# Optimization experiments

Hardware: AMD Instinct MI355X
Metric: run time of the kernel (lower is better)

Reference implementation:

```python
import jax, jax.numpy as jnp
import numpy as np

NC = 80
T0, T1 = 0.0025, 0.0225  # scale_area_thresholds
BOX_W, OBJ_W, CLS_W = 5.0, 1.0, 1.0
BOOST = 2.0  # small_object_boost


def setup_inputs() -> dict:
    key = jax.random.key(0)
    ks = jax.random.split(key, 9)
    B, A, T = 16, 3, 100
    grids = [(80, 80), (40, 40), (20, 20)]
    outs = [jax.random.normal(ks[i], (B, A, h, w, 5 + NC), jnp.float32)
            for i, (h, w) in enumerate(grids)]
    # targets: [B, T, 5] = (x1, y1, x2, y2, class_id) in normalized coords
    cx = jax.random.uniform(ks[3], (B, T), minval=0.05, maxval=0.95)
    cy = jax.random.uniform(ks[4], (B, T), minval=0.05, maxval=0.95)
    # log-uniform sides -> areas span both thresholds (all 3 scales hit)
    bw = 10.0 ** jax.random.uniform(ks[5], (B, T), minval=-2.3, maxval=-0.6)
    bh = 10.0 ** jax.random.uniform(ks[6], (B, T), minval=-2.3, maxval=-0.6)
    cls_id = jnp.floor(jax.random.uniform(ks[7], (B, T)) * NC)
    targets = jnp.stack([cx - bw / 2, cy - bh / 2, cx + bw / 2, cy + bh / 2, cls_id], axis=-1).astype(jnp.float32)
    return {"out0": outs[0], "out1": outs[1], "out2": outs[2], "targets": targets}


def _bce(logits, t):
    # BCEWithLogits: log(1+e^x) - x*t, numerically stable via logaddexp
    return jnp.logaddexp(0.0, logits) - logits * t


def _iou_xyxy(b1, b2, eps=1e-6):
    x1 = jnp.maximum(b1[..., 0], b2[..., 0]); y1 = jnp.maximum(b1[..., 1], b2[..., 1])
    x2 = jnp.minimum(b1[..., 2], b2[..., 2]); y2 = jnp.minimum(b1[..., 3], b2[..., 3])
    inter = jnp.clip(x2 - x1, 0.0) * jnp.clip(y2 - y1, 0.0)
    a1 = jnp.clip(b1[..., 2] - b1[..., 0], 0.0) * jnp.clip(b1[..., 3] - b1[..., 1], 0.0)
    a2 = jnp.clip(b2[..., 2] - b2[..., 0], 0.0) * jnp.clip(b2[..., 3] - b2[..., 1], 0.0)
    return inter / (a1 + a2 - inter + eps)


def _build_targets(tgts, scale_index, A, H, W):
    """Sequential (order-faithful) scatter of GT boxes onto the grid; vmapped over batch."""
    def per_image(tg):  # tg: [T, 5]
        init = (jnp.zeros((H, W), jnp.float32), jnp.zeros((H, W, 4), jnp.float32),
                jnp.zeros((H, W, NC), jnp.float32), jnp.ones((H, W), jnp.float32))

        def step(carry, t):
            obj, box, cls, w = carry
            x1 = jnp.clip(t[0], 0.0, 1.0); y1 = jnp.clip(t[1], 0.0, 1.0)
            x2 = jnp.clip(t[2], 0.0, 1.0); y2 = jnp.clip(t[3], 0.0, 1.0)
            valid = (x2 > x1) & (y2 > y1)
            area = (x2 - x1) * (y2 - y1)
            sidx = jnp.where(area <= T0, 0, jnp.where(area <= T1, 1, 2))
            valid = valid & (sidx == scale_index)
            gi = jnp.clip(jnp.floor(0.5 * (x1 + x2) * W).astype(jnp.int32), 0, W - 1)
            gj = jnp.clip(jnp.floor(0.5 * (y1 + y2) * H).astype(jnp.int32), 0, H - 1)
            cid = t[4].astype(jnp.int32)
            cls_ok = (cid >= 0) & (cid < NC)
            cidc = jnp.clip(cid, 0, NC - 1)
            smallness = 1.0 - jnp.minimum(1.0, area / max(T0, 1e-6))
            weight = 1.0 + (BOOST - 1.0) * jnp.maximum(0.0, smallness)
            bvec = jnp.stack([x1, y1, x2, y2])
            obj = obj.at[gj, gi].set(jnp.where(valid, 1.0, obj[gj, gi]))
            box = box.at[gj, gi].set(jnp.where(valid, bvec, box[gj, gi]))
            cls = cls.at[gj, gi, cidc].set(jnp.where(valid & cls_ok, 1.0, cls[gj, gi, cidc]))
            w = w.at[gj, gi].set(jnp.where(valid, weight, w[gj, gi]))
            tiny = valid & (area <= T0)
            for dj, di in ((-1, 0), (1, 0), (0, -1), (0, 1)):
                nj, ni = gj + dj, gi + di
                ok = tiny & (nj >= 0) & (nj < H) & (ni >= 0) & (ni < W)
                njc = jnp.clip(nj, 0, H - 1); nic = jnp.clip(ni, 0, W - 1)
                obj = obj.at[njc, nic].set(jnp.where(ok, jnp.maximum(obj[njc, nic], 0.5), obj[njc, nic]))
                box = box.at[njc, nic].set(jnp.where(ok, bvec, box[njc, nic]))
                cls = cls.at[njc, nic, cidc].set(jnp.where(ok & cls_ok, 1.0, cls[njc, nic, cidc]))
                w = w.at[njc, nic].set(jnp.where(ok, jnp.maximum(w[njc, nic], 0.5 * weight), w[njc, nic]))
            return (obj, box, cls, w), None

        (obj, box, cls, w), _ = jax.lax.scan(step, init, tg)
        return obj, box, cls, w

    obj, box, cls, w = jax.vmap(per_image)(tgts)
    B = tgts.shape[0]
    # only anchor 0 is ever assigned (anchor_id = 0 in the original)
    obj_f = jnp.zeros((B, A, H, W), jnp.float32).at[:, 0].set(obj)
    box_f = jnp.zeros((B, A, H, W, 4), jnp.float32).at[:, 0].set(box)
    cls_f = jnp.zeros((B, A, H, W, NC), jnp.float32).at[:, 0].set(cls)
    w_f = jnp.ones((B, A, H, W), jnp.float32).at[:, 0].set(w)
    return obj_f, box_f, cls_f, w_f


def _scale_loss(out, tgts, scale_index):
    B, A, H, W, _ = out.shape
    reg, objp, clsp = out[..., :4], out[..., 4], out[..., 5:]
    obj_t, box_t, cls_t, sw = _build_targets(tgts, scale_index, A, H, W)
    obj_loss = _bce(objp, obj_t).mean()
    pos = obj_t > 0.5
    npos = jnp.sum(pos)
    denom = jnp.maximum(npos, 1).astype(jnp.float32)
    pb = jax.nn.sigmoid(reg)
    d = pb - box_t
    ad = jnp.abs(d)
    l1 = jnp.where(ad < 1.0, 0.5 * d * d, ad - 0.5).mean(-1)  # smooth_l1, beta=1
    box_per = (l1 + 1.0 - _iou_xyxy(pb, box_t)) * sw
    box_loss = jnp.where(npos > 0, jnp.sum(jnp.where(pos, box_per, 0.0)) / denom, 0.0)
    cls_per = _bce(clsp, cls_t).mean(-1) * sw
    cls_loss = jnp.where(npos > 0, jnp.sum(jnp.where(pos, cls_per, 0.0)) / denom, 0.0)
    return box_loss, obj_loss, cls_loss


def reference(out0, out1, out2, targets):
    targets = jax.lax.stop_gradient(targets)  # torch builds targets from python floats (detached)
    outs = (out0, out1, out2)
    bl = ol = cl = 0.0
    for s, o in enumerate(outs):
        b, ob, c = _scale_loss(o, targets, s)
        bl, ol, cl = bl + b, ol + ob, cl + c
    n = float(len(outs))
    bl, ol, cl = bl / n, ol / n, cl / n
    final = BOX_W * bl + OBJ_W * ol + CLS_W * cl
    return final, bl, ol, cl
```

## Files before the change

kernel.cpp:

```cpp
#include <hip/hip_runtime.h>
#include <math.h>

#define NCLS 80
#define NB 16
#define NA 3
#define NT 100

static constexpr int TOTCELLS  = 134400;
static constexpr int CELL_OFF1 = 102400;
static constexpr int CELL_OFF2 = 128000;

static constexpr int OBJ_TOT  = 403200;
static constexpr int OBJ_OFF1 = 307200;
static constexpr int OBJ_OFF2 = 384000;

__device__ unsigned g_lastMain[TOTCELLS];
__device__ unsigned g_lastAny [TOTCELLS];
__device__ unsigned g_maskA   [TOTCELLS*3];
__device__ float4   g_bvec  [NB*NT];
__device__ float    g_weight[NB*NT];
__device__ double   g_objsum[3];
__device__ double   g_boxsum[3];
__device__ double   g_clssum[3];
__device__ unsigned g_npos  [3];
__device__ unsigned g_posCount;
__device__ unsigned g_posList[NB*NT];

__device__ __forceinline__ float softplusf(float x) {
    return fmaxf(x, 0.0f) + log1pf(expf(-fabsf(x)));
}

__global__ __launch_bounds__(256) void k_clear() {
    int i = blockIdx.x * 256 + threadIdx.x;
    g_lastMain[i] = 0u;
    g_lastAny[i]  = 0u;
    g_maskA[3*i+0] = 0u; g_maskA[3*i+1] = 0u; g_maskA[3*i+2] = 0u;
    if (i < 3) { g_objsum[i] = 0.0; g_boxsum[i] = 0.0; g_clssum[i] = 0.0; g_npos[i] = 0u; }
    if (i == 0) g_posCount = 0u;
}

__global__ __launch_bounds__(256) void k_scatter(const float* __restrict__ tgt) {
    int idx = blockIdx.x * 256 + threadIdx.x;
    if (idx >= NB * NT) return;
    int b = idx / NT, t = idx % NT;
    const float* p = tgt + (size_t)idx * 5;
    float x1 = fminf(fmaxf(p[0], 0.0f), 1.0f);
    float y1 = fminf(fmaxf(p[1], 0.0f), 1.0f);
    float x2 = fminf(fmaxf(p[2], 0.0f), 1.0f);
    float y2 = fminf(fmaxf(p[3], 0.0f), 1.0f);
    bool valid = (x2 > x1) && (y2 > y1);
    float area = (x2 - x1) * (y2 - y1);
    int sidx = (area <= 0.0025f) ? 0 : ((area <= 0.0225f) ? 1 : 2);
    int Wd = (sidx == 0) ? 80 : ((sidx == 1) ? 40 : 20);
    int HWc = Wd * Wd;
    int soff = (sidx == 0) ? 0 : ((sidx == 1) ? CELL_OFF1 : CELL_OFF2);

    int gi = (int)floorf(0.5f * (x1 + x2) * (float)Wd);
    int gj = (int)floorf(0.5f * (y1 + y2) * (float)Wd);
    gi = min(max(gi, 0), Wd - 1);
    gj = min(max(gj, 0), Wd - 1);

    int cid = (int)p[4];
    bool cls_ok = (cid >= 0) && (cid < NCLS);
    float smallness = 1.0f - fminf(1.0f, area / 0.0025f);
    float weight = 1.0f + fmaxf(0.0f, smallness);

    g_bvec[idx]   = make_float4(x1, y1, x2, y2);
    g_weight[idx] = weight;

    if (!valid) return;
    unsigned seq = (unsigned)(t + 1);
    int cell = soff + b * HWc + gj * Wd + gi;
    atomicMax(&g_lastMain[cell], seq);
    atomicMax(&g_lastAny[cell],  seq);
    if (cls_ok) atomicOr(&g_maskA[3*cell + (cid >> 5)], 1u << (cid & 31));

    if (area <= 0.0025f) {
        const int dj[4] = {-1, 1, 0, 0};
        const int di[4] = {0, 0, -1, 1};
        #pragma unroll
        for (int k = 0; k < 4; ++k) {
            int nj = gj + dj[k], ni = gi + di[k];
            if (nj >= 0 && nj < Wd && ni >= 0 && ni < Wd) {
                int nc = soff + b * HWc + nj * Wd + ni;
                atomicMax(&g_lastAny[nc], seq);
                if (cls_ok) atomicOr(&g_maskA[3*nc + (cid >> 5)], 1u << (cid & 31));
            }
        }
    }
}

__global__ __launch_bounds__(256) void k_obj(const float* __restrict__ o0,
                                             const float* __restrict__ o1,
                                             const float* __restrict__ o2) {
    __shared__ double sred[256];
    int n = blockIdx.x * 256 + threadIdx.x;
    int s, loc, HW, soff;
    const float* out;
    if (n < OBJ_OFF1)      { s = 0; loc = n;            out = o0; HW = 6400; soff = 0; }
    else if (n < OBJ_OFF2) { s = 1; loc = n - OBJ_OFF1; out = o1; HW = 1600; soff = CELL_OFF1; }
    else                   { s = 2; loc = n - OBJ_OFF2; out = o2; HW = 400;  soff = CELL_OFF2; }
    int b = loc / (NA * HW);
    int r = loc % (NA * HW);
    int a = r / HW;
    int cij = r % HW;

    float x = out[(size_t)loc * 85 + 4];
    float contrib = softplusf(x);
    if (a == 0) {
        int cell = soff + b * HW + cij;
        unsigned lm = g_lastMain[cell];
        float tv = lm ? 1.0f : (g_lastAny[cell] ? 0.5f : 0.0f);
        contrib -= x * tv;
        if (lm) {
            unsigned slot = atomicAdd(&g_posCount, 1u);
            g_posList[slot] = (unsigned)cell;
            atomicAdd(&g_npos[s], 1u);
        }
    }
    sred[threadIdx.x] = (double)contrib;
    __syncthreads();
    for (int st = 128; st > 0; st >>= 1) {
        if (threadIdx.x < st) sred[threadIdx.x] += sred[threadIdx.x + st];
        __syncthreads();
    }
    if (threadIdx.x == 0) atomicAdd(&g_objsum[s], sred[0]);
}

__global__ __launch_bounds__(256) void k_poswork(const float* __restrict__ o0,
                                                 const float* __restrict__ o1,
                                                 const float* __restrict__ o2) {
    __shared__ double sB[4], sC[4];
    __shared__ int    sS[4];
    int wv   = threadIdx.x >> 6;
    int lane = threadIdx.x & 63;
    int w = blockIdx.x * 4 + wv;
    unsigned count = g_posCount;

    double bsum = 0.0, csum = 0.0;
    int sidx = -1;
    if (w < (int)count) {
        int n = (int)g_posList[w];
        int s, b, cij, HW;
        const float* out;
        if (n < CELL_OFF1)      { s = 0; HW = 6400; int l = n;             b = l / 6400; cij = l % 6400; out = o0; }
        else if (n < CELL_OFF2) { s = 1; HW = 1600; int l = n - CELL_OFF1; b = l / 1600; cij = l % 1600; out = o1; }
        else                    { s = 2; HW = 400;  int l = n - CELL_OFF2; b = l / 400;  cij = l % 400;  out = o2; }
        sidx = s;

        const float* base = out + ((size_t)(b * NA * HW) + (size_t)cij) * 85;
        float v0 = base[lane];
        float v1 = (lane < 21) ? base[64 + lane] : 0.0f;

        unsigned m0 = g_maskA[3*n], m1 = g_maskA[3*n+1], m2 = g_maskA[3*n+2];
        unsigned lm = g_lastMain[n], la = g_lastAny[n];
        float4 bt = g_bvec[b * NT + (int)(la - 1u)];
        float  sw = g_weight[b * NT + (int)(lm - 1u)];

        float cl_ = 0.0f;
        if (lane >= 5) {
            int c = lane - 5;
            unsigned bit = ((c < 32) ? (m0 >> c) : (m1 >> (c - 32))) & 1u;
            cl_ += softplusf(v0) - (bit ? v0 : 0.0f);
        }
        if (lane < 21) {
            int c = lane + 59;
            unsigned bit = ((c < 64) ? (m1 >> (c - 32)) : (m2 >> (c - 64))) & 1u;
            cl_ += softplusf(v1) - (bit ? v1 : 0.0f);
        }

        float pv = 1.0f / (1.0f + expf(-v0));
        float pb0 = __shfl(pv, 0), pb1 = __shfl(pv, 1), pb2 = __shfl(pv, 2), pb3 = __shfl(pv, 3);

        #pragma unroll
        for (int off = 32; off > 0; off >>= 1) cl_ += __shfl_xor(cl_, off);

        if (lane == 0) {
            float btv[4] = {bt.x, bt.y, bt.z, bt.w};
            float pb[4]  = {pb0, pb1, pb2, pb3};
            float l1 = 0.0f;
            #pragma unroll
            for (int k = 0; k < 4; ++k) {
                float d = pb[k] - btv[k];
                float ad = fabsf(d);
                l1 += (ad < 1.0f) ? (0.5f * d * d) : (ad - 0.5f);
            }
            l1 *= 0.25f;
            float ix1 = fmaxf(pb0, bt.x), iy1 = fmaxf(pb1, bt.y);
            float ix2 = fminf(pb2, bt.z), iy2 = fminf(pb3, bt.w);
            float inter = fmaxf(ix2 - ix1, 0.0f) * fmaxf(iy2 - iy1, 0.0f);
            float a1 = fmaxf(pb2 - pb0, 0.0f) * fmaxf(pb3 - pb1, 0.0f);
            float a2 = fmaxf(bt.z - bt.x, 0.0f) * fmaxf(bt.w - bt.y, 0.0f);
            float iou = inter / (a1 + a2 - inter + 1e-6f);
            bsum = (double)((l1 + 1.0f - iou) * sw);
            csum = (double)(cl_ * (1.0f / (float)NCLS) * sw);
        }
    }

    if (lane == 0) { sB[wv] = bsum; sC[wv] = csum; sS[wv] = sidx; }
    __syncthreads();
    if (threadIdx.x == 0) {
        double accB[3] = {0.0, 0.0, 0.0};
        double accC[3] = {0.0, 0.0, 0.0};
        #pragma unroll
        for (int i = 0; i < 4; ++i) {
            int si = sS[i];
            if (si >= 0) { accB[si] += sB[i]; accC[si] += sC[i]; }
        }
        #pragma unroll
        for (int s2 = 0; s2 < 3; ++s2) {
            if (accB[s2] != 0.0) atomicAdd(&g_boxsum[s2], accB[s2]);
            if (accC[s2] != 0.0) atomicAdd(&g_clssum[s2], accC[s2]);
        }
    }
}

__global__ void k_final(float* __restrict__ d_out) {
    if (threadIdx.x != 0 || blockIdx.x != 0) return;
    const double cells[3] = {307200.0, 76800.0, 19200.0};
    double bl = 0.0, ol = 0.0, cl = 0.0;
    for (int s = 0; s < 3; ++s) {
        ol += g_objsum[s] / cells[s];
        unsigned np = g_npos[s];
        if (np > 0u) {
            double denom = (double)np;
            bl += g_boxsum[s] / denom;
            cl += g_clssum[s] / denom;
        }
    }
    bl /= 3.0; ol /= 3.0; cl /= 3.0;
    double fin = 5.0 * bl + 1.0 * ol + 1.0 * cl;
    d_out[0] = (float)fin;
    d_out[1] = (float)bl;
    d_out[2] = (float)ol;
    d_out[3] = (float)cl;
}

extern "C" void kernel_launch(void* const* d_in, const int* in_sizes, int n_in,
                              void* d_out, int out_size, void* d_ws, size_t ws_size,
                              hipStream_t stream) {
    const float* o0 = (const float*)d_in[0];
    const float* o1 = (const float*)d_in[1];
    const float* o2 = (const float*)d_in[2];
    const float* tg = (const float*)d_in[3];
    float* outp = (float*)d_out;

    k_clear   <<<TOTCELLS / 256, 256, 0, stream>>>();
    k_scatter <<<(NB * NT + 255) / 256, 256, 0, stream>>>(tg);
    k_obj     <<<OBJ_TOT / 256, 256, 0, stream>>>(o0, o1, o2);
    k_poswork <<<(NB * NT + 3) / 4, 256, 0, stream>>>(o0, o1, o2);
    k_final   <<<1, 64, 0, stream>>>(outp);
}
```

Before: 75.21 us.

## Replace atomic grid scatter with per-image O(T^2) target resolution and two fused kernels

Removes the large cell-state arrays and their clear kernel. Each image's targets are resolved in shared memory by pairwise comparison, which yields winning main cells, neighbor cells, class masks and box records directly. The objectness softplus pass runs in the same launch as target resolution, and target corrections are applied sparsely in the second kernel. Per-block partials plus a last-block reduction replace global double atomics and the final kernel, cutting five launches to two. The cost is quadratic per-image target logic and a more complex completion-counter scheme.

```diff
diff --git a/kernel.cpp b/kernel.cpp
--- a/kernel.cpp
+++ b/kernel.cpp
@@ -6,234 +6,383 @@
 #define NA 3
 #define NT 100
 
-static constexpr int TOTCELLS  = 134400;
-static constexpr int CELL_OFF1 = 102400;
-static constexpr int CELL_OFF2 = 128000;
+static constexpr int SP_BLOCKS  = 800;
+static constexpr int K1_BLOCKS  = NB + SP_BLOCKS;
+static constexpr int POS_BLOCKS = 400;
+static constexpr int NEI_BLOCKS = 16;
+static constexpr int K2_BLOCKS  = POS_BLOCKS + NEI_BLOCKS;
 
 static constexpr int OBJ_TOT  = 403200;
 static constexpr int OBJ_OFF1 = 307200;
 static constexpr int OBJ_OFF2 = 384000;
-
-__device__ unsigned g_lastMain[TOTCELLS];
-__device__ unsigned g_lastAny [TOTCELLS];
-__device__ unsigned g_maskA   [TOTCELLS*3];
-__device__ float4   g_bvec  [NB*NT];
-__device__ float    g_weight[NB*NT];
-__device__ double   g_objsum[3];
-__device__ double   g_boxsum[3];
-__device__ double   g_clssum[3];
-__device__ unsigned g_npos  [3];
-__device__ unsigned g_posCount;
-__device__ unsigned g_posList[NB*NT];
+static constexpr int SP_STRIDE = SP_BLOCKS * 256;
+
+
+__device__ double g_part [SP_BLOCKS][3];
+__device__ int    g_mainCnt[NB];
+__device__ int    g_neiCnt [NB];
+__device__ int    g_recN[NB*NT];
+__device__ float  g_recW[NB*NT];
+__device__ float4 g_recB[NB*NT];
+__device__ uint4  g_recM[NB*NT];
+__device__ int    g_neiList[NB*400];
+__device__ double g_bpart[POS_BLOCKS][3];
+__device__ double g_cpart[POS_BLOCKS][3];
+__device__ double g_opart[POS_BLOCKS][3];
+__device__ double g_ncorrPart[NEI_BLOCKS][3];
+__device__ int    g_nposPart[NB][3];
+__device__ unsigned g_done;
 
 __device__ __forceinline__ float softplusf(float x) {
     return fmaxf(x, 0.0f) + log1pf(expf(-fabsf(x)));
 }
-
-__global__ __launch_bounds__(256) void k_clear() {
-    int i = blockIdx.x * 256 + threadIdx.x;
-    g_lastMain[i] = 0u;
-    g_lastAny[i]  = 0u;
-    g_maskA[3*i+0] = 0u; g_maskA[3*i+1] = 0u; g_maskA[3*i+2] = 0u;
-    if (i < 3) { g_objsum[i] = 0.0; g_boxsum[i] = 0.0; g_clssum[i] = 0.0; g_npos[i] = 0u; }
-    if (i == 0) g_posCount = 0u;
-}
-
-__global__ __launch_bounds__(256) void k_scatter(const float* __restrict__ tgt) {
-    int idx = blockIdx.x * 256 + threadIdx.x;
-    if (idx >= NB * NT) return;
-    int b = idx / NT, t = idx % NT;
-    const float* p = tgt + (size_t)idx * 5;
-    float x1 = fminf(fmaxf(p[0], 0.0f), 1.0f);
-    float y1 = fminf(fmaxf(p[1], 0.0f), 1.0f);
-    float x2 = fminf(fmaxf(p[2], 0.0f), 1.0f);
-    float y2 = fminf(fmaxf(p[3], 0.0f), 1.0f);
-    bool valid = (x2 > x1) && (y2 > y1);
-    float area = (x2 - x1) * (y2 - y1);
-    int sidx = (area <= 0.0025f) ? 0 : ((area <= 0.0225f) ? 1 : 2);
-    int Wd = (sidx == 0) ? 80 : ((sidx == 1) ? 40 : 20);
-    int HWc = Wd * Wd;
-    int soff = (sidx == 0) ? 0 : ((sidx == 1) ? CELL_OFF1 : CELL_OFF2);
-
-    int gi = (int)floorf(0.5f * (x1 + x2) * (float)Wd);
-    int gj = (int)floorf(0.5f * (y1 + y2) * (float)Wd);
-    gi = min(max(gi, 0), Wd - 1);
-    gj = min(max(gj, 0), Wd - 1);
-
-    int cid = (int)p[4];
-    bool cls_ok = (cid >= 0) && (cid < NCLS);
-    float smallness = 1.0f - fminf(1.0f, area / 0.0025f);
-    float weight = 1.0f + fmaxf(0.0f, smallness);
-
-    g_bvec[idx]   = make_float4(x1, y1, x2, y2);
-    g_weight[idx] = weight;
-
-    if (!valid) return;
-    unsigned seq = (unsigned)(t + 1);
-    int cell = soff + b * HWc + gj * Wd + gi;
-    atomicMax(&g_lastMain[cell], seq);
-    atomicMax(&g_lastAny[cell],  seq);
-    if (cls_ok) atomicOr(&g_maskA[3*cell + (cid >> 5)], 1u << (cid & 31));
-
-    if (area <= 0.0025f) {
-        const int dj[4] = {-1, 1, 0, 0};
-        const int di[4] = {0, 0, -1, 1};
+__device__ __forceinline__ double wred64(double v) {
+    #pragma unroll
+    for (int o = 32; o > 0; o >>= 1) v += __shfl_xor(v, o);
+    return v;
+}
+__device__ __forceinline__ int wredi(int v) {
+    #pragma unroll
+    for (int o = 32; o > 0; o >>= 1) v += __shfl_xor(v, o);
+    return v;
+}
+
+__global__ __launch_bounds__(256) void k1(const float* __restrict__ o0,
+                                          const float* __restrict__ o1,
+                                          const float* __restrict__ o2,
+                                          const float* __restrict__ tgt) {
+    int tid = threadIdx.x;
+    if (blockIdx.x < NB) {
+        __shared__ float raw[NT*5];
+        __shared__ int   sCell[NT], sTiny[NT], sCid[NT];
+        __shared__ int   sNc[NT][4];
+        __shared__ float sW[NT];
+        __shared__ float sB4[NT][4];
+        __shared__ int   sCntM, sCntN, sNpos[3];
+        int b = blockIdx.x;
+        for (int j = tid; j < NT*5; j += 256) raw[j] = tgt[b*NT*5 + j];
+        if (tid == 0) { sCntM = 0; sCntN = 0; if (b == 0) g_done = 0u; }
+        if (tid < 3) sNpos[tid] = 0;
+        __syncthreads();
+        if (tid < NT) {
+            int t = tid;
+            const float* p = &raw[t*5];
+            float x1 = fminf(fmaxf(p[0],0.f),1.f);
+            float y1 = fminf(fmaxf(p[1],0.f),1.f);
+            float x2 = fminf(fmaxf(p[2],0.f),1.f);
+            float y2 = fminf(fmaxf(p[3],0.f),1.f);
+            bool valid = (x2 > x1) && (y2 > y1);
+            int cell = -1, tiny = 0;
+            int nc0=-1, nc1=-1, nc2=-1, nc3=-1;
+            float area = 0.f;
+            if (valid) {
+                area = (x2-x1)*(y2-y1);
+                int s  = (area <= 0.0025f) ? 0 : ((area <= 0.0225f) ? 1 : 2);
+                int Wd = (s==0) ? 80 : ((s==1) ? 40 : 20);
+                int LO = (s==0) ? 0  : ((s==1) ? 6400 : 8000);
+                int gi = (int)floorf(0.5f*(x1+x2)*(float)Wd); gi = min(max(gi,0), Wd-1);
+                int gj = (int)floorf(0.5f*(y1+y2)*(float)Wd); gj = min(max(gj,0), Wd-1);
+                cell = LO + gj*Wd + gi;
+                if (area <= 0.0025f) {
+                    tiny = 1;
+                    if (gj-1 >= 0) nc0 = LO + (gj-1)*Wd + gi;
+                    if (gj+1 < Wd) nc1 = LO + (gj+1)*Wd + gi;
+                    if (gi-1 >= 0) nc2 = LO + gj*Wd + gi-1;
+                    if (gi+1 < Wd) nc3 = LO + gj*Wd + gi+1;
+                }
+            }
+            int cid = (int)p[4];
+            bool cls_ok = (cid >= 0) && (cid < NCLS);
+            float smallness = 1.f - fminf(1.f, area / 0.0025f);
+            float w = 1.f + fmaxf(0.f, smallness);
+            sCell[t]=cell; sTiny[t]=tiny;
+            sNc[t][0]=nc0; sNc[t][1]=nc1; sNc[t][2]=nc2; sNc[t][3]=nc3;
+            sCid[t] = cls_ok ? cid : -1;
+            sW[t]=w; sB4[t][0]=x1; sB4[t][1]=y1; sB4[t][2]=x2; sB4[t][3]=y2;
+        }
+        __syncthreads();
+        for (int e = tid; e < NT*5; e += 256) {
+            int t = e / 5, k = e % 5;
+            if (sCell[t] < 0) continue;
+            if (k == 0) {
+                int C = sCell[t];
+                bool lose = false; int la = t;
+                unsigned m0=0, m1=0, m2=0;
+                for (int t2 = 0; t2 < NT; ++t2) {
+                    int c2 = sCell[t2];
+                    if (c2 < 0) continue;
+                    bool isMain = (c2 == C);
+                    if (isMain && t2 > t) { lose = true; break; }
+                    bool touch = isMain;
+                    if (sTiny[t2]) {
+                        #pragma unroll
+                        for (int k2 = 0; k2 < 4; ++k2) touch |= (sNc[t2][k2] == C);
+                    }
+                    if (touch) {
+                        if (t2 > la) la = t2;
+                        int cd = sCid[t2];
+                        if (cd >= 0) {
+                            if (cd < 32) m0 |= 1u << cd;
+                            else if (cd < 64) m1 |= 1u << (cd-32);
+                            else m2 |= 1u << (cd-64);
+                        }
+                    }
+                }
+                if (!lose) {
+                    int slot = atomicAdd(&sCntM, 1);
+                    int s   = (C < 6400) ? 0 : ((C < 8000) ? 1 : 2);
+                    int LO  = (s==0) ? 0 : ((s==1) ? 6400 : 8000);
+                    int HWl = (s==0) ? 6400 : ((s==1) ? 1600 : 400);
+                    int GO  = (s==0) ? 0 : ((s==1) ? 102400 : 128000);
+                    int cij = C - LO;
+                    int gidx = b*NT + slot;
+                    g_recN[gidx] = GO + b*HWl + cij;
+                    g_recW[gidx] = sW[t];
+                    g_recB[gidx] = make_float4(sB4[la][0], sB4[la][1], sB4[la][2], sB4[la][3]);
+                    g_recM[gidx] = make_uint4(m0, m1, m2, 0u);
+                    atomicAdd(&sNpos[s], 1);
+                }
+            } else {
+                if (!sTiny[t]) continue;
+                int C = sNc[t][k-1];
+                if (C < 0) continue;
+                bool dead = false;
+                for (int t2 = 0; t2 < NT; ++t2) {
+                    int c2 = sCell[t2];
+                    if (c2 < 0) continue;
+                    if (c2 == C) { dead = true; break; }
+                    if (t2 > t && sTiny[t2]) {
+                        #pragma unroll
+                        for (int k2 = 0; k2 < 4; ++k2)
+                            if (sNc[t2][k2] == C) dead = true;
+                        if (dead) break;
+                    }
+                }
+                if (!dead) {
+                    int slot = atomicAdd(&sCntN, 1);
+                    int s   = (C < 6400) ? 0 : ((C < 8000) ? 1 : 2);
+                    int LO  = (s==0) ? 0 : ((s==1) ? 6400 : 8000);
+                    int HWl = (s==0) ? 6400 : ((s==1) ? 1600 : 400);
+                    int cij = C - LO;
+                    int elem = b * NA * HWl + cij;
+                    g_neiList[b*400 + slot] = s | (elem << 2);
+                }
+            }
+        }
+        __syncthreads();
+        if (tid == 0) { g_mainCnt[b] = sCntM; g_neiCnt[b] = sCntN; }
+        if (tid < 3)  g_nposPart[b][tid] = sNpos[tid];
+    } else {
+        __shared__ double sw4[4][3];
+        int sb = blockIdx.x - NB;
+        int i0 = sb*256 + tid;
+        double a0 = 0.0, a1 = 0.0, a2 = 0.0;
         #pragma unroll
-        for (int k = 0; k < 4; ++k) {
-            int nj = gj + dj[k], ni = gi + di[k];
-            if (nj >= 0 && nj < Wd && ni >= 0 && ni < Wd) {
-                int nc = soff + b * HWc + nj * Wd + ni;
-                atomicMax(&g_lastAny[nc], seq);
-                if (cls_ok) atomicOr(&g_maskA[3*nc + (cid >> 5)], 1u << (cid & 31));
-            }
+        for (int r = 0; r < 2; ++r) {
+            int n = i0 + r * SP_STRIDE;
+            if (n < OBJ_TOT) {
+                const float* out; int loc, s;
+                if (n < OBJ_OFF1)      { out = o0; loc = n;            s = 0; }
+                else if (n < OBJ_OFF2) { out = o1; loc = n - OBJ_OFF1; s = 1; }
+                else                   { out = o2; loc = n - OBJ_OFF2; s = 2; }
+                double v = (double)softplusf(out[(size_t)loc * 85 + 4]);
+                if (s == 0) a0 += v; else if (s == 1) a1 += v; else a2 += v;
+            }
+        }
+        a0 = wred64(a0); a1 = wred64(a1); a2 = wred64(a2);
+        if ((tid & 63) == 0) { int wv = tid >> 6; sw4[wv][0]=a0; sw4[wv][1]=a1; sw4[wv][2]=a2; }
+        __syncthreads();
+        if (tid == 0) {
+            #pragma unroll
+            for (int s = 0; s < 3; ++s)
+                g_part[sb][s] = sw4[0][s] + sw4[1][s] + sw4[2][s] + sw4[3][s];
         }
     }
 }
 
-__global__ __launch_bounds__(256) void k_obj(const float* __restrict__ o0,
-                                             const float* __restrict__ o1,
-                                             const float* __restrict__ o2) {
-    __shared__ double sred[256];
-    int n = blockIdx.x * 256 + threadIdx.x;
-    int s, loc, HW, soff;
-    const float* out;
-    if (n < OBJ_OFF1)      { s = 0; loc = n;            out = o0; HW = 6400; soff = 0; }
-    else if (n < OBJ_OFF2) { s = 1; loc = n - OBJ_OFF1; out = o1; HW = 1600; soff = CELL_OFF1; }
-    else                   { s = 2; loc = n - OBJ_OFF2; out = o2; HW = 400;  soff = CELL_OFF2; }
-    int b = loc / (NA * HW);
-    int r = loc % (NA * HW);
-    int a = r / HW;
-    int cij = r % HW;
-
-    float x = out[(size_t)loc * 85 + 4];
-    float contrib = softplusf(x);
-    if (a == 0) {
-        int cell = soff + b * HW + cij;
-        unsigned lm = g_lastMain[cell];
-        float tv = lm ? 1.0f : (g_lastAny[cell] ? 0.5f : 0.0f);
-        contrib -= x * tv;
-        if (lm) {
-            unsigned slot = atomicAdd(&g_posCount, 1u);
-            g_posList[slot] = (unsigned)cell;
-            atomicAdd(&g_npos[s], 1u);
+__global__ __launch_bounds__(256) void k2(const float* __restrict__ o0,
+                                          const float* __restrict__ o1,
+                                          const float* __restrict__ o2,
+                                          float* __restrict__ d_out) {
+    int tid = threadIdx.x;
+    if (blockIdx.x < POS_BLOCKS) {
+        __shared__ double sPB[4], sPC[4], sPO[4];
+        __shared__ int    sPS[4];
+        int wv = tid >> 6, lane = tid & 63;
+        int w = blockIdx.x * 4 + wv;
+        int b = w / NT, slot = w % NT;
+        double bsum = 0.0, csum = 0.0, osum = 0.0;
+        int sidx = -1;
+        if (slot < g_mainCnt[b]) {
+            int gidx = b*NT + slot;
+            int n = g_recN[gidx];
+            int s, bb, cij, HW;
+            const float* out;
+            if (n < 102400)      { s=0; HW=6400; int l=n;          bb=l/6400; cij=l%6400; out=o0; }
+            else if (n < 128000) { s=1; HW=1600; int l=n-102400;   bb=l/1600; cij=l%1600; out=o1; }
+            else                 { s=2; HW=400;  int l=n-128000;   bb=l/400;  cij=l%400;  out=o2; }
+            sidx = s;
+            const float* base = out + ((size_t)(bb * NA * HW) + (size_t)cij) * 85;
+            float v0 = base[lane];
+            float v1 = (lane < 21) ? base[64 + lane] : 0.0f;
+
+            uint4  mm = g_recM[gidx];
+            float4 bt = g_recB[gidx];
+            float  sw = g_recW[gidx];
+
+            float cl_ = 0.0f;
+            if (lane >= 5) {
+                int c = lane - 5;
+                unsigned bit = ((c < 32) ? (mm.x >> c) : (mm.y >> (c-32))) & 1u;
+                cl_ += softplusf(v0) - (bit ? v0 : 0.0f);
+            }
+            if (lane < 21) {
+                int c = lane + 59;
+                unsigned bit = ((c < 64) ? (mm.y >> (c-32)) : (mm.z >> (c-64))) & 1u;
+                cl_ += softplusf(v1) - (bit ? v1 : 0.0f);
+            }
+
+            float pv = 1.0f / (1.0f + expf(-v0));
+            float pb0 = __shfl(pv, 0), pb1 = __shfl(pv, 1);
+            float pb2 = __shfl(pv, 2), pb3 = __shfl(pv, 3);
+            float x4  = __shfl(v0, 4);
+
+            #pragma unroll
+            for (int o = 32; o > 0; o >>= 1) cl_ += __shfl_xor(cl_, o);
+
+            if (lane == 0) {
+                float btv[4] = {bt.x, bt.y, bt.z, bt.w};
+                float pb[4]  = {pb0, pb1, pb2, pb3};
+                float l1 = 0.0f;
+                #pragma unroll
+                for (int k = 0; k < 4; ++k) {
+                    float d = pb[k] - btv[k];
+                    float ad = fabsf(d);
+                    l1 += (ad < 1.0f) ? (0.5f*d*d) : (ad - 0.5f);
+                }
+                l1 *= 0.25f;
+                float ix1 = fmaxf(pb0, bt.x), iy1 = fmaxf(pb1, bt.y);
+                float ix2 = fminf(pb2, bt.z), iy2 = fminf(pb3, bt.w);
+                float inter = fmaxf(ix2-ix1, 0.f) * fmaxf(iy2-iy1, 0.f);
+                float a1 = fmaxf(pb2-pb0, 0.f) * fmaxf(pb3-pb1, 0.f);
+                float a2 = fmaxf(bt.z-bt.x, 0.f) * fmaxf(bt.w-bt.y, 0.f);
+                float iou = inter / (a1 + a2 - inter + 1e-6f);
+                bsum = (double)((l1 + 1.0f - iou) * sw);
+                csum = (double)(cl_ * (1.0f / (float)NCLS) * sw);
+                osum = -(double)x4;
+            }
+        }
+        if (lane == 0) { sPB[wv]=bsum; sPC[wv]=csum; sPO[wv]=osum; sPS[wv]=sidx; }
+        __syncthreads();
+        if (tid == 0) {
+            double B0=0,B1=0,B2=0, C0=0,C1=0,C2=0, O0=0,O1=0,O2=0;
+            #pragma unroll
+            for (int i = 0; i < 4; ++i) {
+                int si = sPS[i];
+                if (si == 0)      { B0+=sPB[i]; C0+=sPC[i]; O0+=sPO[i]; }
+                else if (si == 1) { B1+=sPB[i]; C1+=sPC[i]; O1+=sPO[i]; }
+                else if (si == 2) { B2+=sPB[i]; C2+=sPC[i]; O2+=sPO[i]; }
+            }
+            g_bpart[blockIdx.x][0]=B0; g_bpart[blockIdx.x][1]=B1; g_bpart[blockIdx.x][2]=B2;
+            g_cpart[blockIdx.x][0]=C0; g_cpart[blockIdx.x][1]=C1; g_cpart[blockIdx.x][2]=C2;
+            g_opart[blockIdx.x][0]=O0; g_opart[blockIdx.x][1]=O1; g_opart[blockIdx.x][2]=O2;
+        }
+    } else {
+        __shared__ double sN[4][3];
+        int nb = blockIdx.x - POS_BLOCKS;
+        double c0 = 0.0, c1 = 0.0, c2 = 0.0;
+        #pragma unroll
+        for (int r = 0; r < 2; ++r) {
+            int e = nb*256 + tid + r*4096;
+            if (e < NB*400) {
+                int b = e / 400, slot = e % 400;
+                if (slot < g_neiCnt[b]) {
+                    int rec = g_neiList[e];
+                    int s = rec & 3;
+                    int elem = rec >> 2;
+                    const float* out = (s==0) ? o0 : ((s==1) ? o1 : o2);
+                    double v = 0.5 * (double)out[(size_t)elem * 85 + 4];
+                    if (s == 0) c0 -= v; else if (s == 1) c1 -= v; else c2 -= v;
+                }
+            }
+        }
+        c0 = wred64(c0); c1 = wred64(c1); c2 = wred64(c2);
+        if ((tid & 63) == 0) { int wv = tid>>6; sN[wv][0]=c0; sN[wv][1]=c1; sN[wv][2]=c2; }
+        __syncthreads();
+        if (tid == 0) {
+            #pragma unroll
+            for (int s = 0; s < 3; ++s)
+                g_ncorrPart[nb][s] = sN[0][s] + sN[1][s] + sN[2][s] + sN[3][s];
         }
     }
-    sred[threadIdx.x] = (double)contrib;
+
+    __shared__ int sLast;
+    if (tid == 0) {
+        __threadfence();
+        unsigned old = atomicAdd(&g_done, 1u);
+        sLast = (old == (unsigned)(K2_BLOCKS - 1)) ? 1 : 0;
+    }
     __syncthreads();
-    for (int st = 128; st > 0; st >>= 1) {
-        if (threadIdx.x < st) sred[threadIdx.x] += sred[threadIdx.x + st];
-        __syncthreads();
+    if (sLast) {
+        __threadfence();
+        __shared__ double sF[4][12];
+        __shared__ int    sI[4][3];
+        double oS0=0,oS1=0,oS2=0, bS0=0,bS1=0,bS2=0, cS0=0,cS1=0,cS2=0, oC0=0,oC1=0,oC2=0;
+        int n0=0, n1=0, n2=0;
+        for (int r = tid; r < SP_BLOCKS; r += 256) {
+            oS0 += g_part[r][0]; oS1 += g_part[r][1]; oS2 += g_part[r][2];
+        }
+        for (int r = tid; r < POS_BLOCKS; r += 256) {
+            bS0 += g_bpart[r][0]; bS1 += g_bpart[r][1]; bS2 += g_bpart[r][2];
+            cS0 += g_cpart[r][0]; cS1 += g_cpart[r][1]; cS2 += g_cpart[r][2];
+            oC0 += g_opart[r][0]; oC1 += g_opart[r][1]; oC2 += g_opart[r][2];
+        }
+        if (tid < NEI_BLOCKS) {
+            oC0 += g_ncorrPart[tid][0]; oC1 += g_ncorrPart[tid][1]; oC2 += g_ncorrPart[tid][2];
+        }
+        if (tid < NB) {
+            n0 += g_nposPart[tid][0]; n1 += g_nposPart[tid][1]; n2 += g_nposPart[tid][2];
+        }
+        oS0=wred64(oS0); oS1=wred64(oS1); oS2=wred64(oS2);
+        bS0=wred64(bS0); bS1=wred64(bS1); bS2=wred64(bS2);
+        cS0=wred64(cS0); cS1=wred64(cS1); cS2=wred64(cS2);
+        oC0=wred64(oC0); oC1=wred64(oC1); oC2=wred64(oC2);
+        n0=wredi(n0); n1=wredi(n1); n2=wredi(n2);
+        if ((tid & 63) == 0) {
+            int wv = tid >> 6;
+            sF[wv][0]=oS0; sF[wv][1]=oS1; sF[wv][2]=oS2;
+            sF[wv][3]=bS0; sF[wv][4]=bS1; sF[wv][5]=bS2;
+            sF[wv][6]=cS0; sF[wv][7]=cS1; sF[wv][8]=cS2;
+            sF[wv][9]=oC0; sF[wv][10]=oC1; sF[wv][11]=oC2;
+            sI[wv][0]=n0; sI[wv][1]=n1; sI[wv][2]=n2;
+        }
+        __syncthreads();
+        if (tid == 0) {
+            double f[12];
+            #pragma unroll
+            for (int j = 0; j < 12; ++j) f[j] = sF[0][j] + sF[1][j] + sF[2][j] + sF[3][j];
+            int np[3];
+            #pragma unroll
+            for (int s = 0; s < 3; ++s) np[s] = sI[0][s] + sI[1][s] + sI[2][s] + sI[3][s];
+            const double cells[3] = {307200.0, 76800.0, 19200.0};
+            double bl = 0.0, ol = 0.0, cl = 0.0;
+            #pragma unroll
+            for (int s = 0; s < 3; ++s) {
+                ol += (f[s] + f[9+s]) / cells[s];
+                if (np[s] > 0) {
+                    double denom = (double)np[s];
+                    bl += f[3+s] / denom;
+                    cl += f[6+s] / denom;
+                }
+            }
+            bl /= 3.0; ol /= 3.0; cl /= 3.0;
+            double fin = 5.0*bl + 1.0*ol + 1.0*cl;
+            d_out[0] = (float)fin;
+            d_out[1] = (float)bl;
+            d_out[2] = (float)ol;
+            d_out[3] = (float)cl;
+        }
     }
-    if (threadIdx.x == 0) atomicAdd(&g_objsum[s], sred[0]);
-}
-
-__global__ __launch_bounds__(256) void k_poswork(const float* __restrict__ o0,
-                                                 const float* __restrict__ o1,
-                                                 const float* __restrict__ o2) {
-    __shared__ double sB[4], sC[4];
-    __shared__ int    sS[4];
-    int wv   = threadIdx.x >> 6;
-    int lane = threadIdx.x & 63;
-    int w = blockIdx.x * 4 + wv;
-    unsigned count = g_posCount;
-
-    double bsum = 0.0, csum = 0.0;
-    int sidx = -1;
-    if (w < (int)count) {
-        int n = (int)g_posList[w];
-        int s, b, cij, HW;
-        const float* out;
-        if (n < CELL_OFF1)      { s = 0; HW = 6400; int l = n;             b = l / 6400; cij = l % 6400; out = o0; }
-        else if (n < CELL_OFF2) { s = 1; HW = 1600; int l = n - CELL_OFF1; b = l / 1600; cij = l % 1600; out = o1; }
-        else                    { s = 2; HW = 400;  int l = n - CELL_OFF2; b = l / 400;  cij = l % 400;  out = o2; }
-        sidx = s;
-
-        const float* base = out + ((size_t)(b * NA * HW) + (size_t)cij) * 85;
-        float v0 = base[lane];
-        float v1 = (lane < 21) ? base[64 + lane] : 0.0f;
-
-        unsigned m0 = g_maskA[3*n], m1 = g_maskA[3*n+1], m2 = g_maskA[3*n+2];
-        unsigned lm = g_lastMain[n], la = g_lastAny[n];
-        float4 bt = g_bvec[b * NT + (int)(la - 1u)];
-        float  sw = g_weight[b * NT + (int)(lm - 1u)];
-
-        float cl_ = 0.0f;
-        if (lane >= 5) {
-            int c = lane - 5;
-            unsigned bit = ((c < 32) ? (m0 >> c) : (m1 >> (c - 32))) & 1u;
-            cl_ += softplusf(v0) - (bit ? v0 : 0.0f);
-        }
-        if (lane < 21) {
-            int c = lane + 59;
-            unsigned bit = ((c < 64) ? (m1 >> (c - 32)) : (m2 >> (c - 64))) & 1u;
-            cl_ += softplusf(v1) - (bit ? v1 : 0.0f);
-        }
-
-        float pv = 1.0f / (1.0f + expf(-v0));
-        float pb0 = __shfl(pv, 0), pb1 = __shfl(pv, 1), pb2 = __shfl(pv, 2), pb3 = __shfl(pv, 3);
-
-        #pragma unroll
-        for (int off = 32; off > 0; off >>= 1) cl_ += __shfl_xor(cl_, off);
-
-        if (lane == 0) {
-            float btv[4] = {bt.x, bt.y, bt.z, bt.w};
-            float pb[4]  = {pb0, pb1, pb2, pb3};
-            float l1 = 0.0f;
-            #pragma unroll
-            for (int k = 0; k < 4; ++k) {
-                float d = pb[k] - btv[k];
-                float ad = fabsf(d);
-                l1 += (ad < 1.0f) ? (0.5f * d * d) : (ad - 0.5f);
-            }
-            l1 *= 0.25f;
-            float ix1 = fmaxf(pb0, bt.x), iy1 = fmaxf(pb1, bt.y);
-            float ix2 = fminf(pb2, bt.z), iy2 = fminf(pb3, bt.w);
-            float inter = fmaxf(ix2 - ix1, 0.0f) * fmaxf(iy2 - iy1, 0.0f);
-            float a1 = fmaxf(pb2 - pb0, 0.0f) * fmaxf(pb3 - pb1, 0.0f);
-            float a2 = fmaxf(bt.z - bt.x, 0.0f) * fmaxf(bt.w - bt.y, 0.0f);
-            float iou = inter / (a1 + a2 - inter + 1e-6f);
-            bsum = (double)((l1 + 1.0f - iou) * sw);
-            csum = (double)(cl_ * (1.0f / (float)NCLS) * sw);
-        }
-    }
-
-    if (lane == 0) { sB[wv] = bsum; sC[wv] = csum; sS[wv] = sidx; }
-    __syncthreads();
-    if (threadIdx.x == 0) {
-        double accB[3] = {0.0, 0.0, 0.0};
-        double accC[3] = {0.0, 0.0, 0.0};
-        #pragma unroll
-        for (int i = 0; i < 4; ++i) {
-            int si = sS[i];
-            if (si >= 0) { accB[si] += sB[i]; accC[si] += sC[i]; }
-        }
-        #pragma unroll
-        for (int s2 = 0; s2 < 3; ++s2) {
-            if (accB[s2] != 0.0) atomicAdd(&g_boxsum[s2], accB[s2]);
-            if (accC[s2] != 0.0) atomicAdd(&g_clssum[s2], accC[s2]);
-        }
-    }
-}
-
-__global__ void k_final(float* __restrict__ d_out) {
-    if (threadIdx.x != 0 || blockIdx.x != 0) return;
-    const double cells[3] = {307200.0, 76800.0, 19200.0};
-    double bl = 0.0, ol = 0.0, cl = 0.0;
-    for (int s = 0; s < 3; ++s) {
-        ol += g_objsum[s] / cells[s];
-        unsigned np = g_npos[s];
-        if (np > 0u) {
-            double denom = (double)np;
-            bl += g_boxsum[s] / denom;
-            cl += g_clssum[s] / denom;
-        }
-    }
-    bl /= 3.0; ol /= 3.0; cl /= 3.0;
-    double fin = 5.0 * bl + 1.0 * ol + 1.0 * cl;
-    d_out[0] = (float)fin;
-    d_out[1] = (float)bl;
-    d_out[2] = (float)ol;
-    d_out[3] = (float)cl;
 }
 
 extern "C" void kernel_launch(void* const* d_in, const int* in_sizes, int n_in,
@@ -245,9 +394,6 @@
     const float* tg = (const float*)d_in[3];
     float* outp = (float*)d_out;
 
-    k_clear   <<<TOTCELLS / 256, 256, 0, stream>>>();
-    k_scatter <<<(NB * NT + 255) / 256, 256, 0, stream>>>(tg);
-    k_obj     <<<OBJ_TOT / 256, 256, 0, stream>>>(o0, o1, o2);
-    k_poswork <<<(NB * NT + 3) / 4, 256, 0, stream>>>(o0, o1, o2);
-    k_final   <<<1, 64, 0, stream>>>(outp);
-}
+    k1<<<K1_BLOCKS, 256, 0, stream>>>(o0, o1, o2, tg);
+    k2<<<K2_BLOCKS, 256, 0, stream>>>(o0, o1, o2, outp);
+}
```

After: 139.4 us. 85.3% more time.
